# Optimization experiments

Measured on AMD Instinct MI355X. Metric: run time of the kernel, lower is better.

## Reference

```python
import jax, jax.numpy as jnp
import numpy as np

HIDDEN = 1024
HEADS = 16
HEAD_DIM = 64
FFN = 4096
LAYERS = 8
QLEN = 9
PATCH = 4
PREFIX = PATCH + 1
LATENT = 64
NSTEPS = 4


def _rope_tables():
    # matches __init__: cos/sin for positions 0..QLEN-1, sin first half negated
    half = HEAD_DIM // 2
    inv = 1.0 / (10000.0 ** (np.arange(half, dtype=np.float64) / half))
    ang = np.arange(QLEN)[:, None] * inv[None, :]          # [QLEN, half]
    cos = np.concatenate([np.cos(ang), np.cos(ang)], -1)   # [QLEN, HEAD_DIM]
    sin = np.concatenate([-np.sin(ang), np.sin(ang)], -1)  # first half *= -1
    return jnp.asarray(cos, jnp.float32), jnp.asarray(sin, jnp.float32)

ROPE_COS, ROPE_SIN = _rope_tables()


def _rms(x):
    # norm weight * sqrt(hidden) is folded into the following projection
    return x * jax.lax.rsqrt(jnp.sum(x * x, -1, keepdims=True))


def setup_inputs() -> dict:
    key = jax.random.key(0)
    ks = jax.random.split(key, 16)
    s = 0.02
    return {
        "step": 2,
        "random": jax.random.normal(ks[0], (1, PATCH, LATENT), jnp.float32),
        "dit_hidden": jax.random.normal(ks[1], (1, 1, HIDDEN), jnp.float32),
        "feat_cond": jax.random.normal(ks[2], (2, PATCH, HIDDEN), jnp.float32),
        "cfg_value": jnp.array([2.5], jnp.float32),
        "cfg_value_minus": jnp.array([1.0 - 2.5], jnp.float32),
        "t_emb": jax.random.normal(ks[3], (NSTEPS, 1, 1, HIDDEN), jnp.float32) * s,
        "dt": jax.random.uniform(ks[4], (NSTEPS,), jnp.float32) * 0.3,
        "in_proj_w": jax.random.normal(ks[5], (HIDDEN, LATENT), jnp.float32) * s,
        "in_proj_b": jnp.zeros((HIDDEN,), jnp.float32),
        "qkv_w": jax.random.normal(ks[6], (LAYERS, 3 * HIDDEN, HIDDEN), jnp.float32) * s,
        "qkv_b": jnp.zeros((LAYERS, 3 * HIDDEN), jnp.float32),
        "o_w": jax.random.normal(ks[7], (LAYERS, HIDDEN, HIDDEN), jnp.float32) * s,
        "gate_up_w": jax.random.normal(ks[8], (LAYERS, 2 * FFN, HIDDEN), jnp.float32) * s,
        "down_w": jax.random.normal(ks[9], (LAYERS, HIDDEN, FFN), jnp.float32) * s,
        "out_proj_w": jax.random.normal(ks[10], (LATENT, HIDDEN), jnp.float32) * s,
        "out_proj_b": jnp.zeros((LATENT,), jnp.float32),
    }


def reference(step, random, dit_hidden, feat_cond, cfg_value, cfg_value_minus,
              t_emb, dt, in_proj_w, in_proj_b, qkv_w, qkv_b, o_w, gate_up_w,
              down_w, out_proj_w, out_proj_b):
    t = t_emb[step]                                     # [1,1,H]
    h = dit_hidden + t
    h = jnp.concatenate([h, t], 0)                      # [2,1,H]  (cond / uncond)
    x = random @ in_proj_w.T + in_proj_b                # [1,PATCH,H]
    x = jnp.concatenate([x, x], 0)                      # [2,PATCH,H]
    hs = jnp.concatenate([h, feat_cond, x], 1)          # [2,QLEN,H]

    for i in range(LAYERS):
        res = hs
        n = _rms(hs)
        qkv = (n @ qkv_w[i].T + qkv_b[i]).reshape(2, QLEN, 3 * HEADS, HEAD_DIM)
        qk, v = qkv[:, :, :2 * HEADS], qkv[:, :, 2 * HEADS:]
        # RoPE (rotate_half = swap halves; sign is in ROPE_SIN)
        x1, x2 = jnp.split(qk, 2, axis=-1)
        rot = jnp.concatenate([x2, x1], -1)
        qk = qk * ROPE_COS[None, :, None, :] + rot * ROPE_SIN[None, :, None, :]
        q, k = qk[:, :, :HEADS], qk[:, :, HEADS:]
        # head_dim**-0.25 scale already folded into q/k weights
        scores = jnp.einsum('bqhd,bkhd->bhqk', q, k)
        attn = jax.nn.softmax(scores, -1)
        o = jnp.einsum('bhqk,bkhd->bqhd', attn, v).reshape(2, QLEN, HIDDEN)
        hs = res + o @ o_w[i].T
        res = hs
        n = _rms(hs)
        gu = n @ gate_up_w[i].T
        g, u = jnp.split(gu, 2, -1)
        hs = res + (jax.nn.silu(g) * u) @ down_w[i].T

    out = _rms(hs[:, PREFIX:]) @ out_proj_w.T + out_proj_b   # [2,PATCH,LATENT]
    pos = out[:1].reshape(1, 1, -1)
    neg = out[1:].reshape(1, 1, -1)
    dot = jnp.sum(pos * neg, -1, keepdims=True)
    sq = jnp.sum(neg * neg, -1, keepdims=True)
    guided = cfg_value * pos + cfg_value_minus * (dot / sq) * neg
    return random + guided.reshape(1, PATCH, LATENT) * dt[step]
```

## Files before the change

### kernel.cpp

```cpp
#include <hip/hip_runtime.h>
#include <hip/hip_bf16.h>

#define ROWS 18
#define HID 1024

__device__ __forceinline__ float dot4(float4 a, float4 b){
  return fmaf(a.x,b.x, fmaf(a.y,b.y, fmaf(a.z,b.z, a.w*b.w)));
}
__device__ __forceinline__ void fma4(float& acc, float4 w, float4 a){
  acc = fmaf(w.x,a.x, fmaf(w.y,a.y, fmaf(w.z,a.z, fmaf(w.w,a.w, acc))));
}

template<int K, int ASTR, int KB, int PK, int CSTR, bool RMS, bool BIAS, bool ATOMIC, bool SPLITBUF>
__global__ __launch_bounds__(256)
void gemm_k(const float* __restrict__ Wt, const float* __restrict__ act,
            const float* __restrict__ bias, float* __restrict__ outp)
{
  constexpr int NP  = KB / PK;
  constexpr int NCH = PK / 256;
  static_assert(NP <= 2, "");

  __shared__ float sact[ROWS * PK];
  __shared__ float sred[16 * ROWS];
  __shared__ float sscale[ROWS];

  const int tid  = threadIdx.x;
  const int w    = tid >> 6;
  const int lane = tid & 63;
  const int cb   = blockIdx.x * 16;
  const int k0   = blockIdx.y * KB;

  float4 wva[NCH * 4], wvb[NCH * 4];
  float  acc[4][ROWS];
  #pragma unroll
  for (int i = 0; i < 4; i++)
    #pragma unroll
    for (int r = 0; r < ROWS; r++) acc[i][r] = 0.f;

  auto wissue = [&](float4* wv, int p) {
    #pragma unroll
    for (int ch = 0; ch < NCH; ch++)
      #pragma unroll
      for (int i = 0; i < 4; i++)
        wv[ch * 4 + i] = *(const float4*)&Wt[(size_t)(cb + w * 4 + i) * K +
                                             k0 + p * PK + ch * 256 + 4 * lane];
  };
  auto stage = [&](int p) {
    constexpr int N4 = ROWS * PK / 4;
    for (int t4 = tid; t4 < N4; t4 += 256) {
      const int r  = t4 / (PK / 4);
      const int k4 = (t4 % (PK / 4)) * 4;
      *(float4*)&sact[r * PK + k4] =
          *(const float4*)&act[(size_t)r * ASTR + k0 + p * PK + k4];
    }
  };
  auto dofma = [&](const float4* wv) {
    #pragma unroll
    for (int ch = 0; ch < NCH; ch++)
      #pragma unroll
      for (int r = 0; r < ROWS; r++) {
        float4 a = *(const float4*)&sact[r * PK + ch * 256 + 4 * lane];
        #pragma unroll
        for (int i = 0; i < 4; i++) fma4(acc[i][r], wv[ch * 4 + i], a);
      }
  };

  wissue(wva, 0);

  float rs[5] = {0.f,0.f,0.f,0.f,0.f};
  if (RMS) {
    #pragma unroll
    for (int t = 0; t < 5; t++) {
      const int r = w + 4 * t;
      if (r < ROWS) {
        #pragma unroll
        for (int kk = 4 * lane; kk < K; kk += 256) {
          float4 a = *(const float4*)&act[(size_t)r * ASTR + kk];
          rs[t] += dot4(a, a);
        }
      }
    }
  }

  stage(0);
  __syncthreads();
  if (NP > 1) wissue(wvb, 1);
  dofma(wva);
  if (NP > 1) {
    __syncthreads();
    stage(1);
    __syncthreads();
    dofma(wvb);
  }

  if (RMS) {
    #pragma unroll
    for (int t = 0; t < 5; t++) {
      const int r = w + 4 * t;
      if (r < ROWS) {
        float ss = rs[t];
        #pragma unroll
        for (int m = 32; m >= 1; m >>= 1) ss += __shfl_xor(ss, m);
        if (lane == 0) sscale[r] = rsqrtf(ss);
      }
    }
  }

  #pragma unroll
  for (int i = 0; i < 4; i++)
    #pragma unroll
    for (int r = 0; r < ROWS; r++) {
      float v = acc[i][r];
      #pragma unroll
      for (int m = 32; m >= 1; m >>= 1) v += __shfl_xor(v, m);
      if (lane == 0) sred[(w * 4 + i) * ROWS + r] = v;
    }
  __syncthreads();

  float* op = outp + (SPLITBUF ? (size_t)blockIdx.y * ROWS * CSTR : 0);
  for (int t = tid; t < 16 * ROWS; t += 256) {
    const int r    = t % ROWS;
    const int rest = t / ROWS;
    const int c    = cb + rest;
    float v = sred[rest * ROWS + r];
    if (RMS)  v *= sscale[r];
    if (BIAS) { if (blockIdx.y == 0) v += bias[c]; }
    if (ATOMIC) atomicAdd(&op[(size_t)r * CSTR + c], v);
    else        op[(size_t)r * CSTR + c] = v;
  }
}

__global__ __launch_bounds__(512)
void gu_kernel(const float* __restrict__ Wt, const float* __restrict__ act,
               float* __restrict__ gub)
{
  __shared__ float sact[ROWS * 512];
  __shared__ float sred[32 * ROWS];
  __shared__ float sscale[ROWS];

  const int tid  = threadIdx.x;
  const int w    = tid >> 6;
  const int lane = tid & 63;
  const int cb   = blockIdx.x * 16;
  const int wrow0 = (w >= 4 ? 4096 : 0) + cb + (w & 3) * 4;

  float4 wva[8], wvb[8];
  float  acc[4][ROWS];
  #pragma unroll
  for (int i = 0; i < 4; i++)
    #pragma unroll
    for (int r = 0; r < ROWS; r++) acc[i][r] = 0.f;

  auto wissue = [&](float4* wv, int p) {
    #pragma unroll
    for (int ch = 0; ch < 2; ch++)
      #pragma unroll
      for (int i = 0; i < 4; i++)
        wv[ch * 4 + i] = *(const float4*)&Wt[(size_t)(wrow0 + i) * 1024 +
                                             p * 512 + ch * 256 + 4 * lane];
  };
  auto stage = [&](int p) {
    for (int t4 = tid; t4 < ROWS * 128; t4 += 512) {
      const int r  = t4 / 128;
      const int k4 = (t4 % 128) * 4;
      *(float4*)&sact[r * 512 + k4] =
          *(const float4*)&act[(size_t)r * 1024 + p * 512 + k4];
    }
  };
  auto dofma = [&](const float4* wv) {
    #pragma unroll
    for (int ch = 0; ch < 2; ch++)
      #pragma unroll
      for (int r = 0; r < ROWS; r++) {
        float4 a = *(const float4*)&sact[r * 512 + ch * 256 + 4 * lane];
        #pragma unroll
        for (int i = 0; i < 4; i++) fma4(acc[i][r], wv[ch * 4 + i], a);
      }
  };

  wissue(wva, 0);

  float rs[3] = {0.f, 0.f, 0.f};
  #pragma unroll
  for (int t = 0; t < 3; t++) {
    const int r = w + 8 * t;
    if (r < ROWS) {
      #pragma unroll
      for (int kk = 4 * lane; kk < 1024; kk += 256) {
        float4 a = *(const float4*)&act[(size_t)r * 1024 + kk];
        rs[t] += dot4(a, a);
      }
    }
  }

  stage(0);
  __syncthreads();
  wissue(wvb, 1);
  dofma(wva);
  __syncthreads();
  stage(1);
  __syncthreads();
  dofma(wvb);

  #pragma unroll
  for (int t = 0; t < 3; t++) {
    const int r = w + 8 * t;
    if (r < ROWS) {
      float ss = rs[t];
      #pragma unroll
      for (int m = 32; m >= 1; m >>= 1) ss += __shfl_xor(ss, m);
      if (lane == 0) sscale[r] = rsqrtf(ss);
    }
  }

  #pragma unroll
  for (int i = 0; i < 4; i++)
    #pragma unroll
    for (int r = 0; r < ROWS; r++) {
      float v = acc[i][r];
      #pragma unroll
      for (int m = 32; m >= 1; m >>= 1) v += __shfl_xor(v, m);
      if (lane == 0) sred[(w * 4 + i) * ROWS + r] = v;
    }
  __syncthreads();

  for (int t = tid; t < 16 * ROWS; t += 512) {
    const int r = t >> 4;
    const int j = t & 15;
    const float s = sscale[r];
    const float g = sred[j * ROWS + r] * s;
    const float u = sred[(16 + j) * ROWS + r] * s;
    gub[(size_t)r * 4096 + cb + j] = (g / (1.f + __expf(-g))) * u;
  }
}

__global__ __launch_bounds__(256)
void prep_kernel(const int* __restrict__ step, const float* __restrict__ random_,
                 const float* __restrict__ dit_hidden, const float* __restrict__ feat_cond,
                 const float* __restrict__ t_emb, const float* __restrict__ in_w,
                 const float* __restrict__ in_b, float* __restrict__ hs)
{
  const int c = blockIdx.x * 256 + threadIdx.x;
  const int st = step[0];
  const float tv = t_emb[(size_t)st * HID + c];
  hs[0 * HID + c] = dit_hidden[c] + tv;
  hs[9 * HID + c] = tv;
  #pragma unroll
  for (int p = 0; p < 4; p++) {
    hs[(1 + p) * HID + c]  = feat_cond[(size_t)(0 * 4 + p) * HID + c];
    hs[(10 + p) * HID + c] = feat_cond[(size_t)(1 * 4 + p) * HID + c];
  }
  #pragma unroll
  for (int p = 0; p < 4; p++) {
    float a = in_b[c];
    #pragma unroll
    for (int q4 = 0; q4 < 16; q4++) {
      float4 wv = *(const float4*)&in_w[(size_t)c * 64 + q4 * 4];
      float4 rv = *(const float4*)&random_[p * 64 + q4 * 4];
      a += dot4(wv, rv);
    }
    hs[(5 + p) * HID + c]  = a;
    hs[(14 + p) * HID + c] = a;
  }
}

__global__ __launch_bounds__(64)
void attn_kernel(const float* __restrict__ qkvp, float* __restrict__ attn_out)
{
  const int bh = blockIdx.x;
  const int b = bh >> 4, h = bh & 15;
  const int d = threadIdx.x;
  const float* p0 = qkvp + (size_t)b * 9 * 3072;
  const float* p1 = p0 + (size_t)ROWS * 3072;
  float q[9], k[9], v[9];
  #pragma unroll
  for (int i = 0; i < 9; i++) {
    q[i] = p0[i * 3072 + h * 64 + d]        + p1[i * 3072 + h * 64 + d];
    k[i] = p0[i * 3072 + (16 + h) * 64 + d] + p1[i * 3072 + (16 + h) * 64 + d];
    v[i] = p0[i * 3072 + (32 + h) * 64 + d] + p1[i * 3072 + (32 + h) * 64 + d];
  }
  const int j = d & 31;
  const float inv = powf(10000.f, -(float)j * (1.f / 32.f));
  #pragma unroll
  for (int i = 0; i < 9; i++) {
    const float ang = (float)i * inv;
    float sn, cs;
    __sincosf(ang, &sn, &cs);
    const float sgn = (d < 32) ? -sn : sn;
    const float rq = __shfl_xor(q[i], 32);
    const float rk = __shfl_xor(k[i], 32);
    q[i] = q[i] * cs + rq * sgn;
    k[i] = k[i] * cs + rk * sgn;
  }
  float* obase = attn_out + (size_t)b * 9 * HID + h * 64 + d;
  for (int i = 0; i < 9; i++) {
    float sc[9];
    #pragma unroll
    for (int jj = 0; jj < 9; jj++) {
      float p = q[i] * k[jj];
      #pragma unroll
      for (int m = 32; m >= 1; m >>= 1) p += __shfl_xor(p, m);
      sc[jj] = p;
    }
    float mx = sc[0];
    #pragma unroll
    for (int jj = 1; jj < 9; jj++) mx = fmaxf(mx, sc[jj]);
    float den = 0.f;
    #pragma unroll
    for (int jj = 0; jj < 9; jj++) { sc[jj] = __expf(sc[jj] - mx); den += sc[jj]; }
    float o = 0.f;
    #pragma unroll
    for (int jj = 0; jj < 9; jj++) o += sc[jj] * v[jj];
    obase[i * HID] = o / den;
  }
}

__global__ __launch_bounds__(512)
void outcomb_kernel(const float* __restrict__ hs, const float* __restrict__ opw,
                    const float* __restrict__ opb, const float* __restrict__ random_,
                    const float* __restrict__ cfg, const float* __restrict__ cfgm,
                    const float* __restrict__ dt, const int* __restrict__ step,
                    float* __restrict__ dout)
{
  __shared__ float sh[8 * 1024];
  __shared__ float sscale[8];
  __shared__ float sout[512];
  __shared__ float sdot[4], ssq[4];

  const int tid = threadIdx.x;
  const int w = tid >> 6, lane = tid & 63;

  for (int t4 = tid; t4 < 2048; t4 += 512) {
    const int r8 = t4 / 256;
    const int k4 = (t4 % 256) * 4;
    const int row = (r8 >> 2) * 9 + 5 + (r8 & 3);
    *(float4*)&sh[r8 * 1024 + k4] = *(const float4*)&hs[(size_t)row * 1024 + k4];
  }
  __syncthreads();

  {
    float ss = 0.f;
    #pragma unroll
    for (int qq = 0; qq < 4; qq++) {
      float4 a = *(const float4*)&sh[w * 1024 + 4 * lane + 256 * qq];
      ss += dot4(a, a);
    }
    #pragma unroll
    for (int m = 32; m >= 1; m >>= 1) ss += __shfl_xor(ss, m);
    if (lane == 0) sscale[w] = rsqrtf(ss);
  }
  __syncthreads();

  {
    const int r8 = tid & 7;
    const int c  = tid >> 3;
    float a0 = 0.f, a1 = 0.f;
    #pragma unroll 4
    for (int k4 = 0; k4 < 128; k4++) {
      a0 += dot4(*(const float4*)&sh[r8 * 1024 + 8 * k4],
                 *(const float4*)&opw[(size_t)c * 1024 + 8 * k4]);
      a1 += dot4(*(const float4*)&sh[r8 * 1024 + 8 * k4 + 4],
                 *(const float4*)&opw[(size_t)c * 1024 + 8 * k4 + 4]);
    }
    sout[r8 * 64 + c] = (a0 + a1) * sscale[r8] + opb[c];
  }
  __syncthreads();

  float pos = 0.f, neg = 0.f, dd = 0.f, sq = 0.f;
  if (tid < 256) {
    pos = sout[tid]; neg = sout[256 + tid];
    dd = pos * neg; sq = neg * neg;
  }
  #pragma unroll
  for (int m = 32; m >= 1; m >>= 1) { dd += __shfl_xor(dd, m); sq += __shfl_xor(sq, m); }
  if (w < 4 && lane == 0) { sdot[w] = dd; ssq[w] = sq; }
  __syncthreads();
  if (tid < 256) {
    const float dot = sdot[0] + sdot[1] + sdot[2] + sdot[3];
    const float sqs = ssq[0] + ssq[1] + ssq[2] + ssq[3];
    const float guided = cfg[0] * pos + cfgm[0] * (dot / sqs) * neg;
    dout[tid] = random_[tid] + guided * dt[step[0]];
  }
}

extern "C" void kernel_launch(void* const* d_in, const int* in_sizes, int n_in,
                              void* d_out, int out_size, void* d_ws, size_t ws_size,
                              hipStream_t stream)
{
  const int*   step    = (const int*)  d_in[0];
  const float* random_ = (const float*)d_in[1];
  const float* dit_h   = (const float*)d_in[2];
  const float* feat    = (const float*)d_in[3];
  const float* cfg     = (const float*)d_in[4];
  const float* cfgm    = (const float*)d_in[5];
  const float* t_emb   = (const float*)d_in[6];
  const float* dt      = (const float*)d_in[7];
  const float* in_w    = (const float*)d_in[8];
  const float* in_b    = (const float*)d_in[9];
  const float* qkv_w   = (const float*)d_in[10];
  const float* qkv_b   = (const float*)d_in[11];
  const float* o_w     = (const float*)d_in[12];
  const float* gu_w    = (const float*)d_in[13];
  const float* dn_w    = (const float*)d_in[14];
  const float* op_w    = (const float*)d_in[15];
  const float* op_b    = (const float*)d_in[16];

  float* hs    = (float*)d_ws;
  float* qkvp  = hs   + ROWS * HID;
  float* attnb = qkvp + 2 * ROWS * 3072;
  float* gub   = attnb + ROWS * HID;
  float* dout  = (float*)d_out;

  prep_kernel<<<4, 256, 0, stream>>>(step, random_, dit_h, feat, t_emb, in_w, in_b, hs);

  for (int i = 0; i < 8; i++) {
    const float* qw = qkv_w + (size_t)i * 3072 * 1024;
    const float* qb = qkv_b + (size_t)i * 3072;
    const float* ow = o_w   + (size_t)i * 1024 * 1024;
    const float* gw = gu_w  + (size_t)i * 8192 * 1024;
    const float* dw = dn_w  + (size_t)i * 1024 * 4096;

    gemm_k<1024, 1024, 512, 512, 3072, true, true, false, true>
        <<<dim3(192, 2), 256, 0, stream>>>(qw, hs, qb, qkvp);
    attn_kernel<<<32, 64, 0, stream>>>(qkvp, attnb);
    gemm_k<1024, 1024, 256, 256, 1024, false, false, true, false>
        <<<dim3(64, 4), 256, 0, stream>>>(ow, attnb, nullptr, hs);
    gu_kernel<<<256, 512, 0, stream>>>(gw, hs, gub);
    gemm_k<4096, 4096, 1024, 512, 1024, false, false, true, false>
        <<<dim3(64, 4), 256, 0, stream>>>(dw, gub, nullptr, hs);
  }

  outcomb_kernel<<<1, 512, 0, stream>>>(hs, op_w, op_b, random_, cfg, cfgm, dt,
                                        step, dout);
}
```

Baseline: 948.2 us.

## Replace per-layer kernel launches with one persistent cooperative kernel using grid barriers

All prep, per-layer QKV/attention/O-proj/gate-up/down GEMMs and the output combine now run in a single persistent cooperative kernel of 256 blocks. Stages are separated by atomic-counter grid barriers instead of separate launches. Each block prefetches its next stage's weights into registers before a barrier so the loads overlap the wait. Attention is fused into the O-projection stage. This removes about 40 kernel launch gaps and the split-K partial-buffer sum, but depends on co-residency of all blocks and adds spin-barrier cost and register pressure.

Result: slower. 2.491 ms (+162.7%).

```diff
diff --git a/kernel.cpp b/kernel.cpp
--- a/kernel.cpp
+++ b/kernel.cpp
@@ -1,8 +1,7 @@
 #include <hip/hip_runtime.h>
-#include <hip/hip_bf16.h>
-
+
+#define NBLK 256
 #define ROWS 18
-#define HID 1024
 
 __device__ __forceinline__ float dot4(float4 a, float4 b){
   return fmaf(a.x,b.x, fmaf(a.y,b.y, fmaf(a.z,b.z, a.w*b.w)));
@@ -10,376 +9,378 @@
 __device__ __forceinline__ void fma4(float& acc, float4 w, float4 a){
   acc = fmaf(w.x,a.x, fmaf(w.y,a.y, fmaf(w.z,a.z, fmaf(w.w,a.w, acc))));
 }
-
-template<int K, int ASTR, int KB, int PK, int CSTR, bool RMS, bool BIAS, bool ATOMIC, bool SPLITBUF>
-__global__ __launch_bounds__(256)
-void gemm_k(const float* __restrict__ Wt, const float* __restrict__ act,
-            const float* __restrict__ bias, float* __restrict__ outp)
+__device__ __forceinline__ float wred(float v){
+  #pragma unroll
+  for (int m = 32; m >= 1; m >>= 1) v += __shfl_xor(v, m);
+  return v;
+}
+
+__device__ __forceinline__ void gbar(unsigned* p){
+  __syncthreads();
+  if (threadIdx.x == 0) {
+    __threadfence();
+    __hip_atomic_fetch_add(p, 1u, __ATOMIC_RELAXED, __HIP_MEMORY_SCOPE_AGENT);
+    while (__hip_atomic_load(p, __ATOMIC_RELAXED, __HIP_MEMORY_SCOPE_AGENT) < NBLK)
+      __builtin_amdgcn_s_sleep(2);
+    __threadfence();
+  }
+  __syncthreads();
+}
+
+__global__ __launch_bounds__(512, 2)
+void vox_persist(const int* __restrict__ step, const float* __restrict__ random_,
+                 const float* __restrict__ dit_h, const float* __restrict__ feat,
+                 const float* __restrict__ cfg, const float* __restrict__ cfgm,
+                 const float* __restrict__ t_emb, const float* __restrict__ dt,
+                 const float* __restrict__ in_w, const float* __restrict__ in_b,
+                 const float* __restrict__ qkv_w, const float* __restrict__ qkv_b,
+                 const float* __restrict__ o_w, const float* __restrict__ gu_w,
+                 const float* __restrict__ dn_w, const float* __restrict__ op_w,
+                 const float* __restrict__ op_b,
+                 unsigned* __restrict__ bars,
+                 float* __restrict__ hs, float* __restrict__ qkvb,
+                 float* __restrict__ gub, float* __restrict__ dout)
 {
-  constexpr int NP  = KB / PK;
-  constexpr int NCH = PK / 256;
-  static_assert(NP <= 2, "");
-
-  __shared__ float sact[ROWS * PK];
-  __shared__ float sred[16 * ROWS];
+  __shared__ float sact[ROWS * 1024];
   __shared__ float sscale[ROWS];
-
+  __shared__ float sA[8], sB[8];
+
+  const int b    = blockIdx.x;
   const int tid  = threadIdx.x;
   const int w    = tid >> 6;
   const int lane = tid & 63;
-  const int cb   = blockIdx.x * 16;
-  const int k0   = blockIdx.y * KB;
-
-  float4 wva[NCH * 4], wvb[NCH * 4];
-  float  acc[4][ROWS];
-  #pragma unroll
-  for (int i = 0; i < 4; i++)
+  int bi = 0;
+
+  const float ropeInv = powf(10000.f, -(float)(lane & 31) * (1.f / 32.f));
+
+  float4 wbuf[16];
+
+  if (b < 2) {
+    const int c  = b * 512 + tid;
+    const int st = step[0];
+    const float tv = t_emb[(size_t)st * 1024 + c];
+    hs[0 * 1024 + c] = dit_h[c] + tv;
+    hs[9 * 1024 + c] = tv;
     #pragma unroll
-    for (int r = 0; r < ROWS; r++) acc[i][r] = 0.f;
-
-  auto wissue = [&](float4* wv, int p) {
+    for (int p = 0; p < 4; p++) {
+      hs[(1 + p)  * 1024 + c] = feat[(size_t)(p)     * 1024 + c];
+      hs[(10 + p) * 1024 + c] = feat[(size_t)(4 + p) * 1024 + c];
+    }
     #pragma unroll
-    for (int ch = 0; ch < NCH; ch++)
-      #pragma unroll
-      for (int i = 0; i < 4; i++)
-        wv[ch * 4 + i] = *(const float4*)&Wt[(size_t)(cb + w * 4 + i) * K +
-                                             k0 + p * PK + ch * 256 + 4 * lane];
+    for (int p = 0; p < 4; p++) {
+      float a = in_b[c];
+      #pragma unroll
+      for (int q4 = 0; q4 < 16; q4++) {
+        float4 wv = *(const float4*)&in_w[(size_t)c * 64 + q4 * 4];
+        float4 rv = *(const float4*)&random_[p * 64 + q4 * 4];
+        a += dot4(wv, rv);
+      }
+      hs[(5 + p)  * 1024 + c] = a;
+      hs[(14 + p) * 1024 + c] = a;
+    }
+  }
+
+  const int cbq = 12 * b;
+  const int cg  = b & 63, ky = b >> 6;
+  const int cbo = 16 * cg;
+  const int cbg = 16 * b;
+  const int cbd = 16 * cg;
+
+  auto stage = [&](const float* src, int stride, int koff) {
+    #pragma unroll
+    for (int t = 0; t < 9; t++) {
+      const int t4 = t * 512 + tid;
+      const int r  = t4 >> 8;
+      const int k4 = (t4 & 255) * 4;
+      *(float4*)&sact[r * 1024 + k4] = *(const float4*)&src[(size_t)r * stride + koff + k4];
+    }
   };
-  auto stage = [&](int p) {
-    constexpr int N4 = ROWS * PK / 4;
-    for (int t4 = tid; t4 < N4; t4 += 256) {
-      const int r  = t4 / (PK / 4);
-      const int k4 = (t4 % (PK / 4)) * 4;
-      *(float4*)&sact[r * PK + k4] =
-          *(const float4*)&act[(size_t)r * ASTR + k0 + p * PK + k4];
-    }
-  };
-  auto dofma = [&](const float4* wv) {
+
+  {
+    const float* qw = qkv_w;
+    if (w < 6) {
+      #pragma unroll
+      for (int c = 0; c < 2; c++)
+        #pragma unroll
+        for (int ch = 0; ch < 4; ch++)
+          wbuf[c * 4 + ch] = *(const float4*)&qw[(size_t)(cbq + 2 * w + c) * 1024 + ch * 256 + 4 * lane];
+    }
+  }
+  gbar(&bars[(bi++) * 16]);
+
+  for (int l = 0; l < 8; l++) {
+    const float* qb = qkv_b + (size_t)l * 3072;
+    const float* ow = o_w   + (size_t)l * 1024 * 1024;
+    const float* gw = gu_w  + (size_t)l * 8192 * 1024;
+    const float* dw = dn_w  + (size_t)l * 1024 * 4096;
+
+    {
+      stage(hs, 1024, 0);
+      __syncthreads();
+      if (w >= 6) {
+        #pragma unroll
+        for (int t = 0; t < 9; t++) {
+          const int r = (w - 6) * 9 + t;
+          float ss = 0.f;
+          #pragma unroll
+          for (int q = 0; q < 4; q++) {
+            float4 a = *(const float4*)&sact[r * 1024 + q * 256 + 4 * lane];
+            ss += dot4(a, a);
+          }
+          ss = wred(ss);
+          if (lane == 0) sscale[r] = rsqrtf(ss);
+        }
+      }
+      float acc[2][ROWS];
+      if (w < 6) {
+        #pragma unroll
+        for (int c = 0; c < 2; c++)
+          #pragma unroll
+          for (int r = 0; r < ROWS; r++) acc[c][r] = 0.f;
+        #pragma unroll
+        for (int ch = 0; ch < 4; ch++)
+          #pragma unroll
+          for (int r = 0; r < ROWS; r++) {
+            float4 a = *(const float4*)&sact[r * 1024 + ch * 256 + 4 * lane];
+            fma4(acc[0][r], wbuf[ch], a);
+            fma4(acc[1][r], wbuf[4 + ch], a);
+          }
+      }
+      __syncthreads();
+      if (w < 6) {
+        #pragma unroll
+        for (int c = 0; c < 2; c++)
+          #pragma unroll
+          for (int r = 0; r < ROWS; r++) {
+            float v = wred(acc[c][r]);
+            if (lane == 0) {
+              const int col = cbq + 2 * w + c;
+              qkvb[r * 3072 + col] = v * sscale[r] + qb[col];
+            }
+          }
+      }
+    }
     #pragma unroll
-    for (int ch = 0; ch < NCH; ch++)
+    for (int c = 0; c < 2; c++)
+      wbuf[c] = *(const float4*)&ow[(size_t)(cbo + 2 * w + c) * 1024 + ky * 256 + 4 * lane];
+    gbar(&bars[(bi++) * 16]);
+
+    {
+      const int bb = w >> 2, hw = w & 3, h = 4 * ky + hw;
+      float q[9], k[9], v[9];
+      #pragma unroll
+      for (int i = 0; i < 9; i++) {
+        const float* base = qkvb + (size_t)(bb * 9 + i) * 3072;
+        q[i] = base[h * 64 + lane];
+        k[i] = base[1024 + h * 64 + lane];
+        v[i] = base[2048 + h * 64 + lane];
+      }
+      #pragma unroll
+      for (int i = 0; i < 9; i++) {
+        const float ang = (float)i * ropeInv;
+        float sn, cs;
+        __sincosf(ang, &sn, &cs);
+        const float sgn = (lane < 32) ? -sn : sn;
+        const float rq = __shfl_xor(q[i], 32);
+        const float rk = __shfl_xor(k[i], 32);
+        q[i] = q[i] * cs + rq * sgn;
+        k[i] = k[i] * cs + rk * sgn;
+      }
+      #pragma unroll
+      for (int i = 0; i < 9; i++) {
+        float sc[9];
+        #pragma unroll
+        for (int jj = 0; jj < 9; jj++) sc[jj] = wred(q[i] * k[jj]);
+        float mx = sc[0];
+        #pragma unroll
+        for (int jj = 1; jj < 9; jj++) mx = fmaxf(mx, sc[jj]);
+        float den = 0.f;
+        #pragma unroll
+        for (int jj = 0; jj < 9; jj++) { sc[jj] = __expf(sc[jj] - mx); den += sc[jj]; }
+        float o = 0.f;
+        #pragma unroll
+        for (int jj = 0; jj < 9; jj++) o += sc[jj] * v[jj];
+        sact[(bb * 9 + i) * 256 + hw * 64 + lane] = o / den;
+      }
+      __syncthreads();
+      float acc[2][ROWS];
+      #pragma unroll
+      for (int c = 0; c < 2; c++)
+        #pragma unroll
+        for (int r = 0; r < ROWS; r++) acc[c][r] = 0.f;
       #pragma unroll
       for (int r = 0; r < ROWS; r++) {
-        float4 a = *(const float4*)&sact[r * PK + ch * 256 + 4 * lane];
-        #pragma unroll
-        for (int i = 0; i < 4; i++) fma4(acc[i][r], wv[ch * 4 + i], a);
-      }
-  };
-
-  wissue(wva, 0);
-
-  float rs[5] = {0.f,0.f,0.f,0.f,0.f};
-  if (RMS) {
+        float4 a = *(const float4*)&sact[r * 256 + 4 * lane];
+        fma4(acc[0][r], wbuf[0], a);
+        fma4(acc[1][r], wbuf[1], a);
+      }
+      #pragma unroll
+      for (int c = 0; c < 2; c++)
+        #pragma unroll
+        for (int r = 0; r < ROWS; r++) {
+          float v2 = wred(acc[c][r]);
+          if (lane == 0) atomicAdd(&hs[r * 1024 + cbo + 2 * w + c], v2);
+        }
+    }
+    {
+      const int c0 = cbg + 2 * w;
+      #pragma unroll
+      for (int j = 0; j < 2; j++)
+        #pragma unroll
+        for (int ch = 0; ch < 4; ch++) {
+          wbuf[j * 4 + ch]     = *(const float4*)&gw[(size_t)(c0 + j) * 1024 + ch * 256 + 4 * lane];
+          wbuf[8 + j * 4 + ch] = *(const float4*)&gw[(size_t)(4096 + c0 + j) * 1024 + ch * 256 + 4 * lane];
+        }
+    }
+    gbar(&bars[(bi++) * 16]);
+
+    {
+      stage(hs, 1024, 0);
+      __syncthreads();
+      #pragma unroll
+      for (int t = 0; t < 3; t++) {
+        const int r = w + 8 * t;
+        if (r < ROWS) {
+          float ss = 0.f;
+          #pragma unroll
+          for (int q = 0; q < 4; q++) {
+            float4 a = *(const float4*)&sact[r * 1024 + q * 256 + 4 * lane];
+            ss += dot4(a, a);
+          }
+          ss = wred(ss);
+          if (lane == 0) sscale[r] = rsqrtf(ss);
+        }
+      }
+      __syncthreads();
+      float acc[4][ROWS];
+      #pragma unroll
+      for (int j = 0; j < 4; j++)
+        #pragma unroll
+        for (int r = 0; r < ROWS; r++) acc[j][r] = 0.f;
+      #pragma unroll
+      for (int ch = 0; ch < 4; ch++)
+        #pragma unroll
+        for (int r = 0; r < ROWS; r++) {
+          float4 a = *(const float4*)&sact[r * 1024 + ch * 256 + 4 * lane];
+          fma4(acc[0][r], wbuf[ch], a);
+          fma4(acc[1][r], wbuf[4 + ch], a);
+          fma4(acc[2][r], wbuf[8 + ch], a);
+          fma4(acc[3][r], wbuf[12 + ch], a);
+        }
+      const int c0 = cbg + 2 * w;
+      #pragma unroll
+      for (int r = 0; r < ROWS; r++) {
+        float g0 = wred(acc[0][r]);
+        float g1 = wred(acc[1][r]);
+        float u0 = wred(acc[2][r]);
+        float u1 = wred(acc[3][r]);
+        if (lane == 0) {
+          const float s = sscale[r];
+          g0 *= s; g1 *= s; u0 *= s; u1 *= s;
+          gub[r * 4096 + c0]     = g0 / (1.f + __expf(-g0)) * u0;
+          gub[r * 4096 + c0 + 1] = g1 / (1.f + __expf(-g1)) * u1;
+        }
+      }
+    }
     #pragma unroll
-    for (int t = 0; t < 5; t++) {
-      const int r = w + 4 * t;
-      if (r < ROWS) {
-        #pragma unroll
-        for (int kk = 4 * lane; kk < K; kk += 256) {
-          float4 a = *(const float4*)&act[(size_t)r * ASTR + kk];
-          rs[t] += dot4(a, a);
-        }
-      }
-    }
+    for (int c = 0; c < 2; c++)
+      #pragma unroll
+      for (int ch = 0; ch < 4; ch++)
+        wbuf[c * 4 + ch] = *(const float4*)&dw[(size_t)(cbd + 2 * w + c) * 4096 + ky * 1024 + ch * 256 + 4 * lane];
+    gbar(&bars[(bi++) * 16]);
+
+    {
+      stage(gub, 4096, ky * 1024);
+      __syncthreads();
+      float acc[2][ROWS];
+      #pragma unroll
+      for (int c = 0; c < 2; c++)
+        #pragma unroll
+        for (int r = 0; r < ROWS; r++) acc[c][r] = 0.f;
+      #pragma unroll
+      for (int ch = 0; ch < 4; ch++)
+        #pragma unroll
+        for (int r = 0; r < ROWS; r++) {
+          float4 a = *(const float4*)&sact[r * 1024 + ch * 256 + 4 * lane];
+          fma4(acc[0][r], wbuf[ch], a);
+          fma4(acc[1][r], wbuf[4 + ch], a);
+        }
+      #pragma unroll
+      for (int c = 0; c < 2; c++)
+        #pragma unroll
+        for (int r = 0; r < ROWS; r++) {
+          float v2 = wred(acc[c][r]);
+          if (lane == 0) atomicAdd(&hs[r * 1024 + cbd + 2 * w + c], v2);
+        }
+    }
+    if (l < 7) {
+      const float* qwn = qkv_w + (size_t)(l + 1) * 3072 * 1024;
+      if (w < 6) {
+        #pragma unroll
+        for (int c = 0; c < 2; c++)
+          #pragma unroll
+          for (int ch = 0; ch < 4; ch++)
+            wbuf[c * 4 + ch] = *(const float4*)&qwn[(size_t)(cbq + 2 * w + c) * 1024 + ch * 256 + 4 * lane];
+      }
+    }
+    gbar(&bars[(bi++) * 16]);
   }
 
-  stage(0);
-  __syncthreads();
-  if (NP > 1) wissue(wvb, 1);
-  dofma(wva);
-  if (NP > 1) {
+  if (b == 0) {
+    for (int t4 = tid; t4 < 2048; t4 += 512) {
+      const int r8 = t4 / 256;
+      const int k4 = (t4 % 256) * 4;
+      const int row = (r8 >> 2) * 9 + 5 + (r8 & 3);
+      *(float4*)&sact[r8 * 1024 + k4] = *(const float4*)&hs[(size_t)row * 1024 + k4];
+    }
     __syncthreads();
-    stage(1);
+    {
+      float ss = 0.f;
+      #pragma unroll
+      for (int qq = 0; qq < 4; qq++) {
+        float4 a = *(const float4*)&sact[w * 1024 + 4 * lane + 256 * qq];
+        ss += dot4(a, a);
+      }
+      ss = wred(ss);
+      if (lane == 0) sA[w] = rsqrtf(ss);
+    }
     __syncthreads();
-    dofma(wvb);
-  }
-
-  if (RMS) {
-    #pragma unroll
-    for (int t = 0; t < 5; t++) {
-      const int r = w + 4 * t;
-      if (r < ROWS) {
-        float ss = rs[t];
-        #pragma unroll
-        for (int m = 32; m >= 1; m >>= 1) ss += __shfl_xor(ss, m);
-        if (lane == 0) sscale[r] = rsqrtf(ss);
-      }
-    }
-  }
-
-  #pragma unroll
-  for (int i = 0; i < 4; i++)
-    #pragma unroll
-    for (int r = 0; r < ROWS; r++) {
-      float v = acc[i][r];
-      #pragma unroll
-      for (int m = 32; m >= 1; m >>= 1) v += __shfl_xor(v, m);
-      if (lane == 0) sred[(w * 4 + i) * ROWS + r] = v;
-    }
-  __syncthreads();
-
-  float* op = outp + (SPLITBUF ? (size_t)blockIdx.y * ROWS * CSTR : 0);
-  for (int t = tid; t < 16 * ROWS; t += 256) {
-    const int r    = t % ROWS;
-    const int rest = t / ROWS;
-    const int c    = cb + rest;
-    float v = sred[rest * ROWS + r];
-    if (RMS)  v *= sscale[r];
-    if (BIAS) { if (blockIdx.y == 0) v += bias[c]; }
-    if (ATOMIC) atomicAdd(&op[(size_t)r * CSTR + c], v);
-    else        op[(size_t)r * CSTR + c] = v;
-  }
-}
-
-__global__ __launch_bounds__(512)
-void gu_kernel(const float* __restrict__ Wt, const float* __restrict__ act,
-               float* __restrict__ gub)
-{
-  __shared__ float sact[ROWS * 512];
-  __shared__ float sred[32 * ROWS];
-  __shared__ float sscale[ROWS];
-
-  const int tid  = threadIdx.x;
-  const int w    = tid >> 6;
-  const int lane = tid & 63;
-  const int cb   = blockIdx.x * 16;
-  const int wrow0 = (w >= 4 ? 4096 : 0) + cb + (w & 3) * 4;
-
-  float4 wva[8], wvb[8];
-  float  acc[4][ROWS];
-  #pragma unroll
-  for (int i = 0; i < 4; i++)
-    #pragma unroll
-    for (int r = 0; r < ROWS; r++) acc[i][r] = 0.f;
-
-  auto wissue = [&](float4* wv, int p) {
-    #pragma unroll
-    for (int ch = 0; ch < 2; ch++)
-      #pragma unroll
-      for (int i = 0; i < 4; i++)
-        wv[ch * 4 + i] = *(const float4*)&Wt[(size_t)(wrow0 + i) * 1024 +
-                                             p * 512 + ch * 256 + 4 * lane];
-  };
-  auto stage = [&](int p) {
-    for (int t4 = tid; t4 < ROWS * 128; t4 += 512) {
-      const int r  = t4 / 128;
-      const int k4 = (t4 % 128) * 4;
-      *(float4*)&sact[r * 512 + k4] =
-          *(const float4*)&act[(size_t)r * 1024 + p * 512 + k4];
-    }
-  };
-  auto dofma = [&](const float4* wv) {
-    #pragma unroll
-    for (int ch = 0; ch < 2; ch++)
-      #pragma unroll
-      for (int r = 0; r < ROWS; r++) {
-        float4 a = *(const float4*)&sact[r * 512 + ch * 256 + 4 * lane];
-        #pragma unroll
-        for (int i = 0; i < 4; i++) fma4(acc[i][r], wv[ch * 4 + i], a);
-      }
-  };
-
-  wissue(wva, 0);
-
-  float rs[3] = {0.f, 0.f, 0.f};
-  #pragma unroll
-  for (int t = 0; t < 3; t++) {
-    const int r = w + 8 * t;
-    if (r < ROWS) {
-      #pragma unroll
-      for (int kk = 4 * lane; kk < 1024; kk += 256) {
-        float4 a = *(const float4*)&act[(size_t)r * 1024 + kk];
-        rs[t] += dot4(a, a);
-      }
-    }
-  }
-
-  stage(0);
-  __syncthreads();
-  wissue(wvb, 1);
-  dofma(wva);
-  __syncthreads();
-  stage(1);
-  __syncthreads();
-  dofma(wvb);
-
-  #pragma unroll
-  for (int t = 0; t < 3; t++) {
-    const int r = w + 8 * t;
-    if (r < ROWS) {
-      float ss = rs[t];
-      #pragma unroll
-      for (int m = 32; m >= 1; m >>= 1) ss += __shfl_xor(ss, m);
-      if (lane == 0) sscale[r] = rsqrtf(ss);
-    }
-  }
-
-  #pragma unroll
-  for (int i = 0; i < 4; i++)
-    #pragma unroll
-    for (int r = 0; r < ROWS; r++) {
-      float v = acc[i][r];
-      #pragma unroll
-      for (int m = 32; m >= 1; m >>= 1) v += __shfl_xor(v, m);
-      if (lane == 0) sred[(w * 4 + i) * ROWS + r] = v;
-    }
-  __syncthreads();
-
-  for (int t = tid; t < 16 * ROWS; t += 512) {
-    const int r = t >> 4;
-    const int j = t & 15;
-    const float s = sscale[r];
-    const float g = sred[j * ROWS + r] * s;
-    const float u = sred[(16 + j) * ROWS + r] * s;
-    gub[(size_t)r * 4096 + cb + j] = (g / (1.f + __expf(-g))) * u;
-  }
-}
-
-__global__ __launch_bounds__(256)
-void prep_kernel(const int* __restrict__ step, const float* __restrict__ random_,
-                 const float* __restrict__ dit_hidden, const float* __restrict__ feat_cond,
-                 const float* __restrict__ t_emb, const float* __restrict__ in_w,
-                 const float* __restrict__ in_b, float* __restrict__ hs)
-{
-  const int c = blockIdx.x * 256 + threadIdx.x;
-  const int st = step[0];
-  const float tv = t_emb[(size_t)st * HID + c];
-  hs[0 * HID + c] = dit_hidden[c] + tv;
-  hs[9 * HID + c] = tv;
-  #pragma unroll
-  for (int p = 0; p < 4; p++) {
-    hs[(1 + p) * HID + c]  = feat_cond[(size_t)(0 * 4 + p) * HID + c];
-    hs[(10 + p) * HID + c] = feat_cond[(size_t)(1 * 4 + p) * HID + c];
-  }
-  #pragma unroll
-  for (int p = 0; p < 4; p++) {
-    float a = in_b[c];
-    #pragma unroll
-    for (int q4 = 0; q4 < 16; q4++) {
-      float4 wv = *(const float4*)&in_w[(size_t)c * 64 + q4 * 4];
-      float4 rv = *(const float4*)&random_[p * 64 + q4 * 4];
-      a += dot4(wv, rv);
-    }
-    hs[(5 + p) * HID + c]  = a;
-    hs[(14 + p) * HID + c] = a;
-  }
-}
-
-__global__ __launch_bounds__(64)
-void attn_kernel(const float* __restrict__ qkvp, float* __restrict__ attn_out)
-{
-  const int bh = blockIdx.x;
-  const int b = bh >> 4, h = bh & 15;
-  const int d = threadIdx.x;
-  const float* p0 = qkvp + (size_t)b * 9 * 3072;
-  const float* p1 = p0 + (size_t)ROWS * 3072;
-  float q[9], k[9], v[9];
-  #pragma unroll
-  for (int i = 0; i < 9; i++) {
-    q[i] = p0[i * 3072 + h * 64 + d]        + p1[i * 3072 + h * 64 + d];
-    k[i] = p0[i * 3072 + (16 + h) * 64 + d] + p1[i * 3072 + (16 + h) * 64 + d];
-    v[i] = p0[i * 3072 + (32 + h) * 64 + d] + p1[i * 3072 + (32 + h) * 64 + d];
-  }
-  const int j = d & 31;
-  const float inv = powf(10000.f, -(float)j * (1.f / 32.f));
-  #pragma unroll
-  for (int i = 0; i < 9; i++) {
-    const float ang = (float)i * inv;
-    float sn, cs;
-    __sincosf(ang, &sn, &cs);
-    const float sgn = (d < 32) ? -sn : sn;
-    const float rq = __shfl_xor(q[i], 32);
-    const float rk = __shfl_xor(k[i], 32);
-    q[i] = q[i] * cs + rq * sgn;
-    k[i] = k[i] * cs + rk * sgn;
-  }
-  float* obase = attn_out + (size_t)b * 9 * HID + h * 64 + d;
-  for (int i = 0; i < 9; i++) {
-    float sc[9];
-    #pragma unroll
-    for (int jj = 0; jj < 9; jj++) {
-      float p = q[i] * k[jj];
-      #pragma unroll
-      for (int m = 32; m >= 1; m >>= 1) p += __shfl_xor(p, m);
-      sc[jj] = p;
-    }
-    float mx = sc[0];
-    #pragma unroll
-    for (int jj = 1; jj < 9; jj++) mx = fmaxf(mx, sc[jj]);
-    float den = 0.f;
-    #pragma unroll
-    for (int jj = 0; jj < 9; jj++) { sc[jj] = __expf(sc[jj] - mx); den += sc[jj]; }
-    float o = 0.f;
-    #pragma unroll
-    for (int jj = 0; jj < 9; jj++) o += sc[jj] * v[jj];
-    obase[i * HID] = o / den;
-  }
-}
-
-__global__ __launch_bounds__(512)
-void outcomb_kernel(const float* __restrict__ hs, const float* __restrict__ opw,
-                    const float* __restrict__ opb, const float* __restrict__ random_,
-                    const float* __restrict__ cfg, const float* __restrict__ cfgm,
-                    const float* __restrict__ dt, const int* __restrict__ step,
-                    float* __restrict__ dout)
-{
-  __shared__ float sh[8 * 1024];
-  __shared__ float sscale[8];
-  __shared__ float sout[512];
-  __shared__ float sdot[4], ssq[4];
-
-  const int tid = threadIdx.x;
-  const int w = tid >> 6, lane = tid & 63;
-
-  for (int t4 = tid; t4 < 2048; t4 += 512) {
-    const int r8 = t4 / 256;
-    const int k4 = (t4 % 256) * 4;
-    const int row = (r8 >> 2) * 9 + 5 + (r8 & 3);
-    *(float4*)&sh[r8 * 1024 + k4] = *(const float4*)&hs[(size_t)row * 1024 + k4];
-  }
-  __syncthreads();
-
-  {
-    float ss = 0.f;
-    #pragma unroll
-    for (int qq = 0; qq < 4; qq++) {
-      float4 a = *(const float4*)&sh[w * 1024 + 4 * lane + 256 * qq];
-      ss += dot4(a, a);
-    }
-    #pragma unroll
-    for (int m = 32; m >= 1; m >>= 1) ss += __shfl_xor(ss, m);
-    if (lane == 0) sscale[w] = rsqrtf(ss);
-  }
-  __syncthreads();
-
-  {
-    const int r8 = tid & 7;
-    const int c  = tid >> 3;
-    float a0 = 0.f, a1 = 0.f;
-    #pragma unroll 4
-    for (int k4 = 0; k4 < 128; k4++) {
-      a0 += dot4(*(const float4*)&sh[r8 * 1024 + 8 * k4],
-                 *(const float4*)&opw[(size_t)c * 1024 + 8 * k4]);
-      a1 += dot4(*(const float4*)&sh[r8 * 1024 + 8 * k4 + 4],
-                 *(const float4*)&opw[(size_t)c * 1024 + 8 * k4 + 4]);
-    }
-    sout[r8 * 64 + c] = (a0 + a1) * sscale[r8] + opb[c];
-  }
-  __syncthreads();
-
-  float pos = 0.f, neg = 0.f, dd = 0.f, sq = 0.f;
-  if (tid < 256) {
-    pos = sout[tid]; neg = sout[256 + tid];
-    dd = pos * neg; sq = neg * neg;
-  }
-  #pragma unroll
-  for (int m = 32; m >= 1; m >>= 1) { dd += __shfl_xor(dd, m); sq += __shfl_xor(sq, m); }
-  if (w < 4 && lane == 0) { sdot[w] = dd; ssq[w] = sq; }
-  __syncthreads();
-  if (tid < 256) {
-    const float dot = sdot[0] + sdot[1] + sdot[2] + sdot[3];
-    const float sqs = ssq[0] + ssq[1] + ssq[2] + ssq[3];
-    const float guided = cfg[0] * pos + cfgm[0] * (dot / sqs) * neg;
-    dout[tid] = random_[tid] + guided * dt[step[0]];
+    float outv[1];
+    {
+      const int r8 = tid & 7;
+      const int c  = tid >> 3;
+      float a0 = 0.f, a1 = 0.f;
+      #pragma unroll 4
+      for (int k4 = 0; k4 < 128; k4++) {
+        a0 += dot4(*(const float4*)&sact[r8 * 1024 + 8 * k4],
+                   *(const float4*)&op_w[(size_t)c * 1024 + 8 * k4]);
+        a1 += dot4(*(const float4*)&sact[r8 * 1024 + 8 * k4 + 4],
+                   *(const float4*)&op_w[(size_t)c * 1024 + 8 * k4 + 4]);
+      }
+      outv[0] = (a0 + a1) * sA[r8] + op_b[c];
+    }
+    __syncthreads();
+    {
+      const int r8 = tid & 7;
+      const int c  = tid >> 3;
+      sact[r8 * 64 + c] = outv[0];
+    }
+    __syncthreads();
+    float pos = 0.f, neg = 0.f, dd = 0.f, sq = 0.f;
+    if (tid < 256) {
+      pos = sact[tid]; neg = sact[256 + tid];
+      dd = pos * neg; sq = neg * neg;
+    }
+    dd = wred(dd); sq = wred(sq);
+    if (lane == 0) { sA[w] = dd; sB[w] = sq; }
+    __syncthreads();
+    if (tid < 256) {
+      float dot = 0.f, sqs = 0.f;
+      #pragma unroll
+      for (int jj = 0; jj < 8; jj++) { dot += sA[jj]; sqs += sB[jj]; }
+      const float guided = cfg[0] * pos + cfgm[0] * (dot / sqs) * neg;
+      dout[tid] = random_[tid] + guided * dt[step[0]];
+    }
   }
 }
 
@@ -405,31 +406,21 @@
   const float* op_w    = (const float*)d_in[15];
   const float* op_b    = (const float*)d_in[16];
 
-  float* hs    = (float*)d_ws;
-  float* qkvp  = hs   + ROWS * HID;
-  float* attnb = qkvp + 2 * ROWS * 3072;
-  float* gub   = attnb + ROWS * HID;
-  float* dout  = (float*)d_out;
-
-  prep_kernel<<<4, 256, 0, stream>>>(step, random_, dit_h, feat, t_emb, in_w, in_b, hs);
-
-  for (int i = 0; i < 8; i++) {
-    const float* qw = qkv_w + (size_t)i * 3072 * 1024;
-    const float* qb = qkv_b + (size_t)i * 3072;
-    const float* ow = o_w   + (size_t)i * 1024 * 1024;
-    const float* gw = gu_w  + (size_t)i * 8192 * 1024;
-    const float* dw = dn_w  + (size_t)i * 1024 * 4096;
-
-    gemm_k<1024, 1024, 512, 512, 3072, true, true, false, true>
-        <<<dim3(192, 2), 256, 0, stream>>>(qw, hs, qb, qkvp);
-    attn_kernel<<<32, 64, 0, stream>>>(qkvp, attnb);
-    gemm_k<1024, 1024, 256, 256, 1024, false, false, true, false>
-        <<<dim3(64, 4), 256, 0, stream>>>(ow, attnb, nullptr, hs);
-    gu_kernel<<<256, 512, 0, stream>>>(gw, hs, gub);
-    gemm_k<4096, 4096, 1024, 512, 1024, false, false, true, false>
-        <<<dim3(64, 4), 256, 0, stream>>>(dw, gub, nullptr, hs);
-  }
-
-  outcomb_kernel<<<1, 512, 0, stream>>>(hs, op_w, op_b, random_, cfg, cfgm, dt,
-                                        step, dout);
-}
+  unsigned* bars = (unsigned*)d_ws;
+  float* hs   = (float*)((char*)d_ws + 4096);
+  float* qkvb = hs + ROWS * 1024;
+  float* gub  = qkvb + ROWS * 3072;
+  float* dout = (float*)d_out;
+
+  hipMemsetAsync(d_ws, 0, 4096, stream);
+
+  void* args[] = {
+    (void*)&step, (void*)&random_, (void*)&dit_h, (void*)&feat, (void*)&cfg,
+    (void*)&cfgm, (void*)&t_emb, (void*)&dt, (void*)&in_w, (void*)&in_b,
+    (void*)&qkv_w, (void*)&qkv_b, (void*)&o_w, (void*)&gu_w, (void*)&dn_w,
+    (void*)&op_w, (void*)&op_b, (void*)&bars,
+    (void*)&hs, (void*)&qkvb, (void*)&gub, (void*)&dout
+  };
+  hipLaunchCooperativeKernel((void*)vox_persist, dim3(NBLK), dim3(512),
+                             args, 0, stream);
+}
```
